# Kernel tuning notes

Measured on AMD Instinct MI355X. Metric: run time of the kernel, lower is better.

## Reference

```python
import jax, jax.numpy as jnp
import numpy as np

V, E, L = 32000, 512, 2  # vocab_size, n_embd (== hidden), n_layer
B, T = 8, 1024


def setup_inputs() -> dict:
    key = jax.random.key(0)
    ks = jax.random.split(key, 6)
    inp = jax.random.randint(ks[0], (B, T), 0, V)
    wte = jax.random.normal(ks[1], (V, E), dtype=jnp.float32) * 0.02
    # PyTorch LSTM params per layer: weight_ih [4H, in], weight_hh [4H, H], b_ih [4H], b_hh [4H]
    W_ih = jax.random.normal(ks[2], (L, 4 * E, E), dtype=jnp.float32) * 0.04
    W_hh = jax.random.normal(ks[3], (L, 4 * E, E), dtype=jnp.float32) * 0.04
    b_ih = jnp.zeros((L, 4 * E), dtype=jnp.float32)
    b_hh = jnp.zeros((L, 4 * E), dtype=jnp.float32)
    fc_w = jax.random.normal(ks[4], (V, E), dtype=jnp.float32) * 0.02
    fc_b = jnp.zeros((V,), dtype=jnp.float32)
    return {"inp": inp, "wte": wte, "W_ih": W_ih, "W_hh": W_hh,
            "b_ih": b_ih, "b_hh": b_hh, "fc_w": fc_w, "fc_b": fc_b}


def _lstm_stack(x, W_ih, W_hh, b_ih, b_hh):
    # x: [B, T, E]; multi-layer LSTM, zero initial (h, c), PyTorch gate order i,f,g,o
    H = W_hh.shape[-1]
    n_layers = W_ih.shape[0]
    for l in range(n_layers):
        # input-to-hidden part is time-parallel: precompute once per layer
        xg = jnp.einsum('bte,ge->btg', x, W_ih[l]) + b_ih[l] + b_hh[l]  # [B,T,4H]
        Whh = W_hh[l]
        h0 = jnp.zeros((x.shape[0], H), x.dtype)
        c0 = jnp.zeros((x.shape[0], H), x.dtype)

        def step(carry, xg_t, Whh=Whh):
            h, c = carry
            g = xg_t + h @ Whh.T  # [B,4H]
            i, f, gg, o = jnp.split(g, 4, axis=-1)
            c = jax.nn.sigmoid(f) * c + jax.nn.sigmoid(i) * jnp.tanh(gg)
            h = jax.nn.sigmoid(o) * jnp.tanh(c)
            return (h, c), h

        (_, _), hs = jax.lax.scan(step, (h0, c0), jnp.swapaxes(xg, 0, 1))  # hs: [T,B,H]
        x = jnp.swapaxes(hs, 0, 1)  # [B,T,H] feeds next layer
    return x


def reference(inp, wte, W_ih, W_hh, b_ih, b_hh, fc_w, fc_b):
    x = wte[inp]  # [B,T,E] embedding lookup
    h = _lstm_stack(x, W_ih, W_hh, b_ih, b_hh)  # [B,T,H]
    logits = jnp.einsum('bth,vh->btv', h, fc_w) + fc_b  # [B,T,V]
    return logits
```

## Files before the change

kernel.cpp:

```cpp
#include <hip/hip_runtime.h>
#include <stdint.h>

typedef __attribute__((ext_vector_type(4))) float f32x4;
typedef __attribute__((ext_vector_type(8))) short s16x8;
typedef __attribute__((ext_vector_type(4))) unsigned short u16x4;
typedef __attribute__((ext_vector_type(4))) unsigned int u32x4;

#define T_SEQ 1024
#define HID 512

__device__ __forceinline__ unsigned short f2bf(float f) {
  uint32_t u = __float_as_uint(f);
  u += 0x7fffu + ((u >> 16) & 1u);
  return (unsigned short)(u >> 16);
}
__device__ __forceinline__ float sigf(float x) { return 1.f / (1.f + __expf(-x)); }
__device__ __forceinline__ float tanhfast(float x) {
  float e = __expf(2.f * x);
  return (e - 1.f) / (e + 1.f);
}

#define ASTORE(p, v) __hip_atomic_store((p), (v), __ATOMIC_RELAXED, __HIP_MEMORY_SCOPE_AGENT)
#define MFMA(a, b, c) __builtin_amdgcn_mfma_f32_16x16x32_bf16((a), (b), (c), 0, 0, 0)

__device__ __forceinline__ u32x4 load_coh16(const unsigned int* p) {
  u32x4 r;
  asm volatile("global_load_dwordx4 %0, %1, off sc0 sc1" : "=v"(r) : "v"(p) : "memory");
  return r;
}
#define VM_WAIT0 do { asm volatile("s_waitcnt vmcnt(0)" ::: "memory"); \
                      __builtin_amdgcn_sched_barrier(0); } while (0)

#define GLL(gp, lp)                                                      \
  __builtin_amdgcn_global_load_lds(                                     \
      (const __attribute__((address_space(1))) void*)(gp),              \
      (__attribute__((address_space(3))) void*)(lp), 16, 0, 0)

__global__ __launch_bounds__(256) void embed_kernel(const int* __restrict__ inp,
                                                    const float* __restrict__ wte,
                                                    unsigned short* __restrict__ xbf) {
  const int m = blockIdx.x;
  const int idx = inp[m];
  const float* src = wte + (size_t)idx * HID;
  unsigned short* dst = xbf + (size_t)m * HID;
  const int e = threadIdx.x;
  dst[e] = f2bf(src[e]);
  dst[e + 256] = f2bf(src[e + 256]);
}

__global__ __launch_bounds__(256) void cvt_bf16_kernel(const float* __restrict__ src,
                                                       unsigned short* __restrict__ dst,
                                                       int n4) {
  const int i = blockIdx.x * 256 + threadIdx.x;
  if (i >= n4) return;
  f32x4 v = ((const f32x4*)src)[i];
  u16x4 o;
  o.x = f2bf(v.x); o.y = f2bf(v.y); o.z = f2bf(v.z); o.w = f2bf(v.w);
  ((u16x4*)dst)[i] = o;
}

__global__ __launch_bounds__(256) void bias_sum_kernel(const float* __restrict__ a,
                                                       const float* __restrict__ b,
                                                       float* __restrict__ o, int n) {
  const int i = blockIdx.x * 256 + threadIdx.x;
  if (i < n) o[i] = a[i] + b[i];
}

template <int MODE>
__global__ __launch_bounds__(256) void gemm_bt(const unsigned short* __restrict__ A,
                                               const unsigned short* __restrict__ B,
                                               float* __restrict__ C,
                                               const float* __restrict__ bias,
                                               int M, int N, int K) {
  __shared__ unsigned short As[128 * 32];
  __shared__ unsigned short Bs[128 * 32];
  const int nTiles = N >> 7;
  const int mt = blockIdx.x / nTiles;
  const int nt = blockIdx.x - mt * nTiles;
  const int m0 = mt << 7, n0 = nt << 7;
  const int tid = threadIdx.x;
  const int wave = tid >> 6, lane = tid & 63;
  const int wm = wave >> 1, wn = wave & 1;

  const int c1 = wave * 64 + lane;
  const int c2 = 256 + c1;
  const unsigned short* gA1 = A + (size_t)(m0 + (c1 >> 2)) * K + (c1 & 3) * 8;
  const unsigned short* gA2 = A + (size_t)(m0 + (c2 >> 2)) * K + (c2 & 3) * 8;
  const unsigned short* gB1 = B + (size_t)(n0 + (c1 >> 2)) * K + (c1 & 3) * 8;
  const unsigned short* gB2 = B + (size_t)(n0 + (c2 >> 2)) * K + (c2 & 3) * 8;
  unsigned short* lA1 = As + wave * 512;
  unsigned short* lA2 = As + 2048 + wave * 512;
  unsigned short* lB1 = Bs + wave * 512;
  unsigned short* lB2 = Bs + 2048 + wave * 512;

  f32x4 acc[4][4] = {};
  const int row_lo = lane & 15;
  const int kq = (lane >> 4) * 8;

  for (int k0 = 0; k0 < K; k0 += 32) {
    GLL(gA1 + k0, lA1);
    GLL(gA2 + k0, lA2);
    GLL(gB1 + k0, lB1);
    GLL(gB2 + k0, lB2);
    __syncthreads();
    s16x8 af[4], bfr[4];
#pragma unroll
    for (int f = 0; f < 4; ++f) {
      af[f] = *(const s16x8*)(As + (wm * 64 + f * 16 + row_lo) * 32 + kq);
      bfr[f] = *(const s16x8*)(Bs + (wn * 64 + f * 16 + row_lo) * 32 + kq);
    }
#pragma unroll
    for (int i = 0; i < 4; ++i)
#pragma unroll
      for (int j = 0; j < 4; ++j)
        acc[i][j] = MFMA(af[i], bfr[j], acc[i][j]);
    __syncthreads();
  }

  float bv[4];
#pragma unroll
  for (int j = 0; j < 4; ++j) bv[j] = bias[n0 + wn * 64 + j * 16 + row_lo];
  const int rbase = (lane >> 4) * 4;
#pragma unroll
  for (int i = 0; i < 4; ++i) {
#pragma unroll
    for (int r = 0; r < 4; ++r) {
      const int m = m0 + wm * 64 + i * 16 + rbase + r;
      const size_t row = MODE == 1 ? ((size_t)(m & 7) * T_SEQ + (m >> 3)) : (size_t)m;
      float* cp = C + row * (size_t)N;
#pragma unroll
      for (int j = 0; j < 4; ++j) cp[n0 + wn * 64 + j * 16 + row_lo] = acc[i][j][r] + bv[j];
    }
  }
}

__global__ __launch_bounds__(256, 1) void lstm_fused(
    const float* __restrict__ xg1,
    const unsigned short* __restrict__ whh1,
    const unsigned short* __restrict__ wih2,
    const unsigned short* __restrict__ whh2,
    const float* __restrict__ bias2,
    unsigned int* __restrict__ h1T,
    unsigned int* __restrict__ h2T,
    unsigned short* __restrict__ h2out) {
  __shared__ __align__(16) char lds1[2][8192];
  __shared__ __align__(16) char lds2[8192];
  __shared__ float GT1[512];
  __shared__ float GT2[512];

  const int tid = threadIdx.x;
  const int wg = blockIdx.x;
  const int g = tid >> 6, l = tid & 63;
  const int unit = l & 15, grp = l >> 4;
  const int u0 = wg * 16;
  const int row = l & 7;

  s16x8 b1[16], b2i[16], b2h[16];
  {
    const size_t grow = (size_t)(g * 512 + u0 + unit) * 512;
#pragma unroll
    for (int kt = 0; kt < 16; ++kt) {
      b1[kt] = *(const s16x8*)(whh1 + grow + kt * 32 + grp * 8);
      b2i[kt] = *(const s16x8*)(wih2 + grow + kt * 32 + grp * 8);
      b2h[kt] = *(const s16x8*)(whh2 + grow + kt * 32 + grp * 8);
    }
  }

  const int pb = l & 7, pu = l >> 3;
  float bias_g[2][4];
  if (g == 0) {
#pragma unroll
    for (int r = 0; r < 2; ++r)
#pragma unroll
      for (int gg = 0; gg < 4; ++gg)
        bias_g[r][gg] = bias2[gg * 512 + u0 + r * 8 + pu];
  }
  float c1a = 0.f, c1b = 0.f, c2a = 0.f, c2b = 0.f;

  const int sr = tid & 7, sc = tid >> 3;
  const int so0 = (sr * 1024 + sc * 32) ^ (sr << 4);
  const int so1 = (sr * 1024 + sc * 32 + 16) ^ (sr << 4);
  const int srcoff = sr * 512 + sc * 16;

  for (int t = 0; t <= T_SEQ + 1; ++t) {
    const int cur = t & 1;

    float xv[2][4];
    if (g == 0 && t < T_SEQ) {
#pragma unroll
      for (int r = 0; r < 2; ++r)
#pragma unroll
        for (int gg = 0; gg < 4; ++gg)
          xv[r][gg] = xg1[((size_t)pb * T_SEQ + t) * 2048 + gg * 512 + u0 + r * 8 + pu];
    }

    const bool need1 = (t >= 1) && (t <= T_SEQ);
    const bool need2 = (t >= 3);
    if (need1 || need2) {
      const unsigned int* s1 = h1T + (size_t)(t - 1) * 4096 + srcoff;
      const unsigned int* s2 = h2T + (size_t)(t - 3) * 4096 + srcoff;
      const unsigned int tg1 = (unsigned int)t, tg2 = (unsigned int)(t - 2);
      u32x4 d0 = {}, d1 = {}, d2 = {}, d3 = {}, e0 = {}, e1 = {}, e2 = {}, e3 = {};
      int spin = 0;
      for (;;) {
        if (need1) {
          d0 = load_coh16(s1); d1 = load_coh16(s1 + 4);
          d2 = load_coh16(s1 + 8); d3 = load_coh16(s1 + 12);
        }
        if (need2) {
          e0 = load_coh16(s2); e1 = load_coh16(s2 + 4);
          e2 = load_coh16(s2 + 8); e3 = load_coh16(s2 + 12);
        }
        VM_WAIT0;
        bool ok = true;
        if (need1) {
#pragma unroll
          for (int j = 0; j < 4; ++j) {
            ok &= (d0[j] >> 16) == tg1; ok &= (d1[j] >> 16) == tg1;
            ok &= (d2[j] >> 16) == tg1; ok &= (d3[j] >> 16) == tg1;
          }
        }
        if (need2) {
#pragma unroll
          for (int j = 0; j < 4; ++j) {
            ok &= (e0[j] >> 16) == tg2; ok &= (e1[j] >> 16) == tg2;
            ok &= (e2[j] >> 16) == tg2; ok &= (e3[j] >> 16) == tg2;
          }
        }
        if (__ballot(ok) == ~0ULL) break;
        if (++spin > (1 << 14)) break;
        __builtin_amdgcn_s_sleep(1);
      }
      if (need1) {
        *(u32x4*)(lds1[cur] + so0) =
            u32x4{(d0[0] & 0xffffu) | (d0[1] << 16), (d0[2] & 0xffffu) | (d0[3] << 16),
                  (d1[0] & 0xffffu) | (d1[1] << 16), (d1[2] & 0xffffu) | (d1[3] << 16)};
        *(u32x4*)(lds1[cur] + so1) =
            u32x4{(d2[0] & 0xffffu) | (d2[1] << 16), (d2[2] & 0xffffu) | (d2[3] << 16),
                  (d3[0] & 0xffffu) | (d3[1] << 16), (d3[2] & 0xffffu) | (d3[3] << 16)};
      }
      if (need2) {
        *(u32x4*)(lds2 + so0) =
            u32x4{(e0[0] & 0xffffu) | (e0[1] << 16), (e0[2] & 0xffffu) | (e0[3] << 16),
                  (e1[0] & 0xffffu) | (e1[1] << 16), (e1[2] & 0xffffu) | (e1[3] << 16)};
        *(u32x4*)(lds2 + so1) =
            u32x4{(e2[0] & 0xffffu) | (e2[1] << 16), (e2[2] & 0xffffu) | (e2[3] << 16),
                  (e3[0] & 0xffffu) | (e3[1] << 16), (e3[2] & 0xffffu) | (e3[3] << 16)};
      }
    }
    if (t == 0) {
      *(u32x4*)(lds1[0] + so0) = u32x4{0, 0, 0, 0};
      *(u32x4*)(lds1[0] + so1) = u32x4{0, 0, 0, 0};
    }
    if (t == 2) {
      *(u32x4*)(lds2 + so0) = u32x4{0, 0, 0, 0};
      *(u32x4*)(lds2 + so1) = u32x4{0, 0, 0, 0};
    }
    __syncthreads();

    if (t < T_SEQ) {
      const char* hb = lds1[cur];
      f32x4 q0 = {}, q1 = {}, q2 = {}, q3 = {};
#pragma unroll
      for (int kt = 0; kt < 16; kt += 4) {
        s16x8 x0 = *(const s16x8*)(hb + ((row * 1024 + (kt + 0) * 64 + grp * 16) ^ (row << 4)));
        s16x8 x1 = *(const s16x8*)(hb + ((row * 1024 + (kt + 1) * 64 + grp * 16) ^ (row << 4)));
        s16x8 x2 = *(const s16x8*)(hb + ((row * 1024 + (kt + 2) * 64 + grp * 16) ^ (row << 4)));
        s16x8 x3 = *(const s16x8*)(hb + ((row * 1024 + (kt + 3) * 64 + grp * 16) ^ (row << 4)));
        q0 = MFMA(x0, b1[kt + 0], q0);
        q1 = MFMA(x1, b1[kt + 1], q1);
        q2 = MFMA(x2, b1[kt + 2], q2);
        q3 = MFMA(x3, b1[kt + 3], q3);
      }
      f32x4 acc = (q0 + q1) + (q2 + q3);
      if (grp < 2) *(f32x4*)(GT1 + g * 128 + unit * 8 + grp * 4) = acc;
    }
    __syncthreads();

    if (g == 0 && t < T_SEQ) {
#pragma unroll
      for (int r = 0; r < 2; ++r) {
        const int u = r * 8 + pu;
        float gi = GT1[0 + u * 8 + pb] + xv[r][0];
        float gf = GT1[128 + u * 8 + pb] + xv[r][1];
        float gv = GT1[256 + u * 8 + pb] + xv[r][2];
        float go = GT1[384 + u * 8 + pb] + xv[r][3];
        float& cc = r ? c1b : c1a;
        cc = sigf(gf) * cc + sigf(gi) * tanhfast(gv);
        const float hv = sigf(go) * tanhfast(cc);
        ASTORE(h1T + (size_t)t * 4096 + pb * 512 + u0 + u,
               (unsigned int)f2bf(hv) | ((unsigned int)(t + 1) << 16));
      }
    }

    if (t >= 2) {
      const char* ha = lds1[cur ^ 1];
      f32x4 q0 = {}, q1 = {}, q2 = {}, q3 = {};
#pragma unroll
      for (int kt = 0; kt < 16; kt += 4) {
        s16x8 x0 = *(const s16x8*)(ha + ((row * 1024 + (kt + 0) * 64 + grp * 16) ^ (row << 4)));
        s16x8 x1 = *(const s16x8*)(ha + ((row * 1024 + (kt + 1) * 64 + grp * 16) ^ (row << 4)));
        s16x8 x2 = *(const s16x8*)(ha + ((row * 1024 + (kt + 2) * 64 + grp * 16) ^ (row << 4)));
        s16x8 x3 = *(const s16x8*)(ha + ((row * 1024 + (kt + 3) * 64 + grp * 16) ^ (row << 4)));
        q0 = MFMA(x0, b2i[kt + 0], q0);
        q1 = MFMA(x1, b2i[kt + 1], q1);
        q2 = MFMA(x2, b2i[kt + 2], q2);
        q3 = MFMA(x3, b2i[kt + 3], q3);
      }
#pragma unroll
      for (int kt = 0; kt < 16; kt += 4) {
        s16x8 x0 = *(const s16x8*)(lds2 + ((row * 1024 + (kt + 0) * 64 + grp * 16) ^ (row << 4)));
        s16x8 x1 = *(const s16x8*)(lds2 + ((row * 1024 + (kt + 1) * 64 + grp * 16) ^ (row << 4)));
        s16x8 x2 = *(const s16x8*)(lds2 + ((row * 1024 + (kt + 2) * 64 + grp * 16) ^ (row << 4)));
        s16x8 x3 = *(const s16x8*)(lds2 + ((row * 1024 + (kt + 3) * 64 + grp * 16) ^ (row << 4)));
        q0 = MFMA(x0, b2h[kt + 0], q0);
        q1 = MFMA(x1, b2h[kt + 1], q1);
        q2 = MFMA(x2, b2h[kt + 2], q2);
        q3 = MFMA(x3, b2h[kt + 3], q3);
      }
      f32x4 acc = (q0 + q1) + (q2 + q3);
      if (grp < 2) *(f32x4*)(GT2 + g * 128 + unit * 8 + grp * 4) = acc;
    }
    __syncthreads();

    if (g == 0 && t >= 2) {
      const int s = t - 2;
#pragma unroll
      for (int r = 0; r < 2; ++r) {
        const int u = r * 8 + pu;
        float gi = GT2[0 + u * 8 + pb] + bias_g[r][0];
        float gf = GT2[128 + u * 8 + pb] + bias_g[r][1];
        float gv = GT2[256 + u * 8 + pb] + bias_g[r][2];
        float go = GT2[384 + u * 8 + pb] + bias_g[r][3];
        float& cc = r ? c2b : c2a;
        cc = sigf(gf) * cc + sigf(gi) * tanhfast(gv);
        const float hv = sigf(go) * tanhfast(cc);
        const unsigned int hb16 = f2bf(hv);
        ASTORE(h2T + (size_t)s * 4096 + pb * 512 + u0 + u,
               hb16 | ((unsigned int)(s + 1) << 16));
        h2out[((size_t)s * 8 + pb) * 512 + u0 + u] = (unsigned short)hb16;
      }
    }
  }
}

extern "C" void kernel_launch(void* const* d_in, const int* in_sizes, int n_in,
                              void* d_out, int out_size, void* d_ws, size_t ws_size,
                              hipStream_t stream) {
  (void)in_sizes; (void)n_in; (void)out_size; (void)ws_size;
  const int* inp = (const int*)d_in[0];
  const float* wte = (const float*)d_in[1];
  const float* W_ih = (const float*)d_in[2];
  const float* W_hh = (const float*)d_in[3];
  const float* b_ih = (const float*)d_in[4];
  const float* b_hh = (const float*)d_in[5];
  const float* fc_w = (const float*)d_in[6];
  const float* fc_b = (const float*)d_in[7];
  float* out = (float*)d_out;

  char* ob = (char*)d_out;
  float* xg1 = (float*)(ob);
  unsigned int* h1T = (unsigned int*)(ob + (64u << 20));
  unsigned int* h2T = (unsigned int*)(ob + (80u << 20));
  unsigned short* x_bf = (unsigned short*)(ob + (96u << 20));
  unsigned short* whh_bf = (unsigned short*)(ob + (104u << 20));
  unsigned short* wih_bf = (unsigned short*)(ob + (108u << 20));

  char* ws = (char*)d_ws;
  unsigned short* fcw_bf = (unsigned short*)(ws);
  float* bias12 = (float*)(ws + (32u << 20));
  unsigned short* h2bf = (unsigned short*)(ws + (35u << 20));

  hipMemsetAsync(ob + (64u << 20), 0, 32u << 20, stream);
  embed_kernel<<<8192, 256, 0, stream>>>(inp, wte, x_bf);
  cvt_bf16_kernel<<<2048, 256, 0, stream>>>(W_ih, wih_bf, 2 * 2048 * 512 / 4);
  cvt_bf16_kernel<<<2048, 256, 0, stream>>>(W_hh, whh_bf, 2 * 2048 * 512 / 4);
  cvt_bf16_kernel<<<16000, 256, 0, stream>>>(fc_w, fcw_bf, 32000 * 512 / 4);
  bias_sum_kernel<<<16, 256, 0, stream>>>(b_ih, b_hh, bias12, 4096);
  gemm_bt<0><<<64 * 16, 256, 0, stream>>>(x_bf, wih_bf, xg1, bias12, 8192, 2048, 512);
  lstm_fused<<<32, 256, 0, stream>>>(xg1, whh_bf, wih_bf + (size_t)2048 * 512,
                                     whh_bf + (size_t)2048 * 512, bias12 + 2048,
                                     h1T, h2T, h2bf);
  gemm_bt<1><<<64 * 250, 256, 0, stream>>>(h2bf, fcw_bf, out, fc_b, 8192, 32000, 512);
}
```

Before: 6.147 ms.

## Warp-specialize fused LSTM kernel with LDS flag handoffs between layer waves

The single lockstep loop over both LSTM layers, with block-wide barriers, becomes a warp-specialized design. Waves 0–1 run layer 1, each computing two gate blocks, and waves 2–3 run layer 2. They hand off through double-buffered LDS tiles and LDS flag counters instead of __syncthreads. Wave 3 prefetches the next layer-1 hidden state while it computes, and the input-projection GEMM now writes a time-major xg layout so the per-step gate loads are contiguous. This is meant to remove the barrier coupling between the layers and to shorten the per-step critical path, at the cost of more spin-polling and of possible deadlock or race hazards in the flag protocol.

```diff
diff --git a/kernel.cpp b/kernel.cpp
--- a/kernel.cpp
+++ b/kernel.cpp
@@ -30,6 +30,23 @@
 }
 #define VM_WAIT0 do { asm volatile("s_waitcnt vmcnt(0)" ::: "memory"); \
                       __builtin_amdgcn_sched_barrier(0); } while (0)
+#define VM_WAIT4 do { asm volatile("s_waitcnt vmcnt(4)" ::: "memory"); \
+                      __builtin_amdgcn_sched_barrier(0); } while (0)
+#define LGKM0 do { asm volatile("s_waitcnt lgkmcnt(0)" ::: "memory"); } while (0)
+
+__device__ __forceinline__ void lds_wait(volatile int* f, int target) {
+  int it = 0;
+  while (*f < target) {
+    if (++it > (1 << 18)) break;
+    __builtin_amdgcn_s_sleep(1);
+  }
+  asm volatile("" ::: "memory");
+}
+
+__device__ __forceinline__ u32x4 pack2(const u32x4 a, const u32x4 b) {
+  return u32x4{(a[0] & 0xffffu) | (a[1] << 16), (a[2] & 0xffffu) | (a[3] << 16),
+               (b[0] & 0xffffu) | (b[1] << 16), (b[2] & 0xffffu) | (b[3] << 16)};
+}
 
 #define GLL(gp, lp)                                                      \
   __builtin_amdgcn_global_load_lds(                                     \
@@ -126,7 +143,9 @@
 #pragma unroll
     for (int r = 0; r < 4; ++r) {
       const int m = m0 + wm * 64 + i * 16 + rbase + r;
-      const size_t row = MODE == 1 ? ((size_t)(m & 7) * T_SEQ + (m >> 3)) : (size_t)m;
+      const size_t row = MODE == 1 ? ((size_t)(m & 7) * T_SEQ + (m >> 3))
+                       : MODE == 2 ? ((size_t)(m & (T_SEQ - 1)) * 8 + (m >> 10))
+                                   : (size_t)m;
       float* cp = C + row * (size_t)N;
 #pragma unroll
       for (int j = 0; j < 4; ++j) cp[n0 + wn * 64 + j * 16 + row_lo] = acc[i][j][r] + bv[j];
@@ -134,8 +153,8 @@
   }
 }
 
-__global__ __launch_bounds__(256, 1) void lstm_fused(
-    const float* __restrict__ xg1,
+__global__ __launch_bounds__(256, 1) void lstm_ws(
+    const float* __restrict__ xg1t,
     const unsigned short* __restrict__ whh1,
     const unsigned short* __restrict__ wih2,
     const unsigned short* __restrict__ whh2,
@@ -143,198 +162,319 @@
     unsigned int* __restrict__ h1T,
     unsigned int* __restrict__ h2T,
     unsigned short* __restrict__ h2out) {
-  __shared__ __align__(16) char lds1[2][8192];
-  __shared__ __align__(16) char lds2[8192];
-  __shared__ float GT1[512];
-  __shared__ float GT2[512];
-
-  const int tid = threadIdx.x;
-  const int wg = blockIdx.x;
-  const int g = tid >> 6, l = tid & 63;
+  __shared__ __align__(16) char t1[2][8192];
+  __shared__ __align__(16) char t1b[2][8192];
+  __shared__ __align__(16) char t2[2][8192];
+  __shared__ float GT1[2][512];
+  __shared__ float GT2[2][512];
+  __shared__ float XG[2][512];
+  __shared__ int F[8];
+
+  const int tid = threadIdx.x, wave = tid >> 6, l = tid & 63;
+  const int wg = blockIdx.x, u0 = wg * 16;
   const int unit = l & 15, grp = l >> 4;
-  const int u0 = wg * 16;
   const int row = l & 7;
-
-  s16x8 b1[16], b2i[16], b2h[16];
-  {
-    const size_t grow = (size_t)(g * 512 + u0 + unit) * 512;
-#pragma unroll
-    for (int kt = 0; kt < 16; ++kt) {
-      b1[kt] = *(const s16x8*)(whh1 + grow + kt * 32 + grp * 8);
-      b2i[kt] = *(const s16x8*)(wih2 + grow + kt * 32 + grp * 8);
-      b2h[kt] = *(const s16x8*)(whh2 + grow + kt * 32 + grp * 8);
-    }
-  }
-
-  const int pb = l & 7, pu = l >> 3;
-  float bias_g[2][4];
-  if (g == 0) {
-#pragma unroll
-    for (int r = 0; r < 2; ++r)
-#pragma unroll
-      for (int gg = 0; gg < 4; ++gg)
-        bias_g[r][gg] = bias2[gg * 512 + u0 + r * 8 + pu];
-  }
-  float c1a = 0.f, c1b = 0.f, c2a = 0.f, c2b = 0.f;
-
-  const int sr = tid & 7, sc = tid >> 3;
-  const int so0 = (sr * 1024 + sc * 32) ^ (sr << 4);
-  const int so1 = (sr * 1024 + sc * 32 + 16) ^ (sr << 4);
-  const int srcoff = sr * 512 + sc * 16;
-
-  for (int t = 0; t <= T_SEQ + 1; ++t) {
-    const int cur = t & 1;
-
-    float xv[2][4];
-    if (g == 0 && t < T_SEQ) {
-#pragma unroll
-      for (int r = 0; r < 2; ++r)
-#pragma unroll
-        for (int gg = 0; gg < 4; ++gg)
-          xv[r][gg] = xg1[((size_t)pb * T_SEQ + t) * 2048 + gg * 512 + u0 + r * 8 + pu];
-    }
-
-    const bool need1 = (t >= 1) && (t <= T_SEQ);
-    const bool need2 = (t >= 3);
-    if (need1 || need2) {
-      const unsigned int* s1 = h1T + (size_t)(t - 1) * 4096 + srcoff;
-      const unsigned int* s2 = h2T + (size_t)(t - 3) * 4096 + srcoff;
-      const unsigned int tg1 = (unsigned int)t, tg2 = (unsigned int)(t - 2);
-      u32x4 d0 = {}, d1 = {}, d2 = {}, d3 = {}, e0 = {}, e1 = {}, e2 = {}, e3 = {};
-      int spin = 0;
-      for (;;) {
-        if (need1) {
-          d0 = load_coh16(s1); d1 = load_coh16(s1 + 4);
-          d2 = load_coh16(s1 + 8); d3 = load_coh16(s1 + 12);
-        }
-        if (need2) {
-          e0 = load_coh16(s2); e1 = load_coh16(s2 + 4);
-          e2 = load_coh16(s2 + 8); e3 = load_coh16(s2 + 12);
-        }
-        VM_WAIT0;
-        bool ok = true;
-        if (need1) {
-#pragma unroll
-          for (int j = 0; j < 4; ++j) {
-            ok &= (d0[j] >> 16) == tg1; ok &= (d1[j] >> 16) == tg1;
-            ok &= (d2[j] >> 16) == tg1; ok &= (d3[j] >> 16) == tg1;
-          }
-        }
-        if (need2) {
-#pragma unroll
-          for (int j = 0; j < 4; ++j) {
-            ok &= (e0[j] >> 16) == tg2; ok &= (e1[j] >> 16) == tg2;
-            ok &= (e2[j] >> 16) == tg2; ok &= (e3[j] >> 16) == tg2;
-          }
-        }
-        if (__ballot(ok) == ~0ULL) break;
-        if (++spin > (1 << 14)) break;
-        __builtin_amdgcn_s_sleep(1);
-      }
-      if (need1) {
-        *(u32x4*)(lds1[cur] + so0) =
-            u32x4{(d0[0] & 0xffffu) | (d0[1] << 16), (d0[2] & 0xffffu) | (d0[3] << 16),
-                  (d1[0] & 0xffffu) | (d1[1] << 16), (d1[2] & 0xffffu) | (d1[3] << 16)};
-        *(u32x4*)(lds1[cur] + so1) =
-            u32x4{(d2[0] & 0xffffu) | (d2[1] << 16), (d2[2] & 0xffffu) | (d2[3] << 16),
-                  (d3[0] & 0xffffu) | (d3[1] << 16), (d3[2] & 0xffffu) | (d3[3] << 16)};
-      }
-      if (need2) {
-        *(u32x4*)(lds2 + so0) =
-            u32x4{(e0[0] & 0xffffu) | (e0[1] << 16), (e0[2] & 0xffffu) | (e0[3] << 16),
-                  (e1[0] & 0xffffu) | (e1[1] << 16), (e1[2] & 0xffffu) | (e1[3] << 16)};
-        *(u32x4*)(lds2 + so1) =
-            u32x4{(e2[0] & 0xffffu) | (e2[1] << 16), (e2[2] & 0xffffu) | (e2[3] << 16),
-                  (e3[0] & 0xffffu) | (e3[1] << 16), (e3[2] & 0xffffu) | (e3[3] << 16)};
-      }
-    }
-    if (t == 0) {
-      *(u32x4*)(lds1[0] + so0) = u32x4{0, 0, 0, 0};
-      *(u32x4*)(lds1[0] + so1) = u32x4{0, 0, 0, 0};
-    }
-    if (t == 2) {
-      *(u32x4*)(lds2 + so0) = u32x4{0, 0, 0, 0};
-      *(u32x4*)(lds2 + so1) = u32x4{0, 0, 0, 0};
-    }
-    __syncthreads();
-
-    if (t < T_SEQ) {
-      const char* hb = lds1[cur];
-      f32x4 q0 = {}, q1 = {}, q2 = {}, q3 = {};
-#pragma unroll
-      for (int kt = 0; kt < 16; kt += 4) {
-        s16x8 x0 = *(const s16x8*)(hb + ((row * 1024 + (kt + 0) * 64 + grp * 16) ^ (row << 4)));
-        s16x8 x1 = *(const s16x8*)(hb + ((row * 1024 + (kt + 1) * 64 + grp * 16) ^ (row << 4)));
-        s16x8 x2 = *(const s16x8*)(hb + ((row * 1024 + (kt + 2) * 64 + grp * 16) ^ (row << 4)));
-        s16x8 x3 = *(const s16x8*)(hb + ((row * 1024 + (kt + 3) * 64 + grp * 16) ^ (row << 4)));
-        q0 = MFMA(x0, b1[kt + 0], q0);
-        q1 = MFMA(x1, b1[kt + 1], q1);
-        q2 = MFMA(x2, b1[kt + 2], q2);
-        q3 = MFMA(x3, b1[kt + 3], q3);
-      }
-      f32x4 acc = (q0 + q1) + (q2 + q3);
-      if (grp < 2) *(f32x4*)(GT1 + g * 128 + unit * 8 + grp * 4) = acc;
-    }
-    __syncthreads();
-
-    if (g == 0 && t < T_SEQ) {
+  const int c64 = l >> 3;
+  volatile int* vF = F;
+
+  if (tid < 8) F[tid] = 0;
+  __syncthreads();
+
+  if (wave == 0) {
+    s16x8 bf[2][16];
+#pragma unroll
+    for (int gi = 0; gi < 2; ++gi) {
+      const size_t grow = (size_t)(gi * 512 + u0 + unit) * 512;
+#pragma unroll
+      for (int kt = 0; kt < 16; ++kt)
+        bf[gi][kt] = *(const s16x8*)(whh1 + grow + kt * 32 + grp * 8);
+    }
+    const int xb = (l >> 1) & 7, xg_ = l >> 4, xh = l & 1;
+    for (int t = 0; t < T_SEQ; ++t) {
+      const int par = t & 1;
+      const float* xs = xg1t + ((size_t)t * 8 + xb) * 2048 + xg_ * 512 + u0 + xh * 8;
+      f32x4 xa = *(const f32x4*)xs;
+      f32x4 xc = *(const f32x4*)(xs + 4);
+      char* dst = t1[par];
+      if (t > 0) {
+        const unsigned int* src = h1T + (size_t)(t - 1) * 4096 + row * 512 + c64 * 64;
+        const unsigned int tg = (unsigned int)t;
+        u32x4 d[16];
+        int spin = 0;
+        for (;;) {
+#pragma unroll
+          for (int j = 0; j < 16; ++j) d[j] = load_coh16(src + j * 4);
+          VM_WAIT0;
+          bool ok = true;
+#pragma unroll
+          for (int j = 0; j < 16; ++j)
+#pragma unroll
+            for (int k = 0; k < 4; ++k) ok &= (d[j][k] >> 16) == tg;
+          if (__ballot(ok) == ~0ULL) break;
+          if (++spin > (1 << 12)) break;
+          __builtin_amdgcn_s_sleep(1);
+        }
+#pragma unroll
+        for (int j2 = 0; j2 < 8; ++j2)
+          *(u32x4*)(dst + ((row * 1024 + c64 * 128 + j2 * 16) ^ (row << 4))) =
+              pack2(d[j2 * 2], d[j2 * 2 + 1]);
+      } else {
+#pragma unroll
+        for (int j2 = 0; j2 < 8; ++j2)
+          *(u32x4*)(dst + ((row * 1024 + c64 * 128 + j2 * 16) ^ (row << 4))) = u32x4{0, 0, 0, 0};
+      }
+      float* xgd = &XG[par][xg_ * 128 + xb * 16 + xh * 8];
+      *(f32x4*)xgd = xa;
+      *(f32x4*)(xgd + 4) = xc;
+      LGKM0;
+      vF[0] = t + 1;
+      const char* hb = t1[par];
+#pragma unroll
+      for (int gi = 0; gi < 2; ++gi) {
+        f32x4 q0 = {}, q1 = {}, q2 = {}, q3 = {};
+#pragma unroll
+        for (int kt = 0; kt < 16; kt += 4) {
+          s16x8 x0 = *(const s16x8*)(hb + ((row * 1024 + (kt + 0) * 64 + grp * 16) ^ (row << 4)));
+          s16x8 x1 = *(const s16x8*)(hb + ((row * 1024 + (kt + 1) * 64 + grp * 16) ^ (row << 4)));
+          s16x8 x2 = *(const s16x8*)(hb + ((row * 1024 + (kt + 2) * 64 + grp * 16) ^ (row << 4)));
+          s16x8 x3 = *(const s16x8*)(hb + ((row * 1024 + (kt + 3) * 64 + grp * 16) ^ (row << 4)));
+          q0 = MFMA(x0, bf[gi][kt + 0], q0);
+          q1 = MFMA(x1, bf[gi][kt + 1], q1);
+          q2 = MFMA(x2, bf[gi][kt + 2], q2);
+          q3 = MFMA(x3, bf[gi][kt + 3], q3);
+        }
+        f32x4 acc = (q0 + q1) + (q2 + q3);
+        if (grp < 2) *(f32x4*)(&GT1[par][gi * 128 + unit * 8 + grp * 4]) = acc;
+      }
+      LGKM0;
+      vF[1] = t + 1;
+    }
+  } else if (wave == 1) {
+    s16x8 bf[2][16];
+#pragma unroll
+    for (int gi = 0; gi < 2; ++gi) {
+      const size_t grow = (size_t)((2 + gi) * 512 + u0 + unit) * 512;
+#pragma unroll
+      for (int kt = 0; kt < 16; ++kt)
+        bf[gi][kt] = *(const s16x8*)(whh1 + grow + kt * 32 + grp * 8);
+    }
+    const int pb = l & 7, pu = l >> 3;
+    float cst[2] = {0.f, 0.f};
+    for (int t = 0; t < T_SEQ; ++t) {
+      const int par = t & 1;
+      lds_wait(&vF[0], t + 1);
+      const char* hb = t1[par];
+#pragma unroll
+      for (int gi = 0; gi < 2; ++gi) {
+        f32x4 q0 = {}, q1 = {}, q2 = {}, q3 = {};
+#pragma unroll
+        for (int kt = 0; kt < 16; kt += 4) {
+          s16x8 x0 = *(const s16x8*)(hb + ((row * 1024 + (kt + 0) * 64 + grp * 16) ^ (row << 4)));
+          s16x8 x1 = *(const s16x8*)(hb + ((row * 1024 + (kt + 1) * 64 + grp * 16) ^ (row << 4)));
+          s16x8 x2 = *(const s16x8*)(hb + ((row * 1024 + (kt + 2) * 64 + grp * 16) ^ (row << 4)));
+          s16x8 x3 = *(const s16x8*)(hb + ((row * 1024 + (kt + 3) * 64 + grp * 16) ^ (row << 4)));
+          q0 = MFMA(x0, bf[gi][kt + 0], q0);
+          q1 = MFMA(x1, bf[gi][kt + 1], q1);
+          q2 = MFMA(x2, bf[gi][kt + 2], q2);
+          q3 = MFMA(x3, bf[gi][kt + 3], q3);
+        }
+        f32x4 acc = (q0 + q1) + (q2 + q3);
+        if (grp < 2) *(f32x4*)(&GT1[par][(2 + gi) * 128 + unit * 8 + grp * 4]) = acc;
+      }
+      lds_wait(&vF[1], t + 1);
 #pragma unroll
       for (int r = 0; r < 2; ++r) {
         const int u = r * 8 + pu;
-        float gi = GT1[0 + u * 8 + pb] + xv[r][0];
-        float gf = GT1[128 + u * 8 + pb] + xv[r][1];
-        float gv = GT1[256 + u * 8 + pb] + xv[r][2];
-        float go = GT1[384 + u * 8 + pb] + xv[r][3];
-        float& cc = r ? c1b : c1a;
-        cc = sigf(gf) * cc + sigf(gi) * tanhfast(gv);
-        const float hv = sigf(go) * tanhfast(cc);
+        float gi = GT1[par][0 + u * 8 + pb] + XG[par][0 + pb * 16 + u];
+        float gf = GT1[par][128 + u * 8 + pb] + XG[par][128 + pb * 16 + u];
+        float gv = GT1[par][256 + u * 8 + pb] + XG[par][256 + pb * 16 + u];
+        float go = GT1[par][384 + u * 8 + pb] + XG[par][384 + pb * 16 + u];
+        cst[r] = sigf(gf) * cst[r] + sigf(gi) * tanhfast(gv);
+        const float hv = sigf(go) * tanhfast(cst[r]);
         ASTORE(h1T + (size_t)t * 4096 + pb * 512 + u0 + u,
                (unsigned int)f2bf(hv) | ((unsigned int)(t + 1) << 16));
       }
     }
-
-    if (t >= 2) {
-      const char* ha = lds1[cur ^ 1];
-      f32x4 q0 = {}, q1 = {}, q2 = {}, q3 = {};
-#pragma unroll
-      for (int kt = 0; kt < 16; kt += 4) {
-        s16x8 x0 = *(const s16x8*)(ha + ((row * 1024 + (kt + 0) * 64 + grp * 16) ^ (row << 4)));
-        s16x8 x1 = *(const s16x8*)(ha + ((row * 1024 + (kt + 1) * 64 + grp * 16) ^ (row << 4)));
-        s16x8 x2 = *(const s16x8*)(ha + ((row * 1024 + (kt + 2) * 64 + grp * 16) ^ (row << 4)));
-        s16x8 x3 = *(const s16x8*)(ha + ((row * 1024 + (kt + 3) * 64 + grp * 16) ^ (row << 4)));
-        q0 = MFMA(x0, b2i[kt + 0], q0);
-        q1 = MFMA(x1, b2i[kt + 1], q1);
-        q2 = MFMA(x2, b2i[kt + 2], q2);
-        q3 = MFMA(x3, b2i[kt + 3], q3);
-      }
-#pragma unroll
-      for (int kt = 0; kt < 16; kt += 4) {
-        s16x8 x0 = *(const s16x8*)(lds2 + ((row * 1024 + (kt + 0) * 64 + grp * 16) ^ (row << 4)));
-        s16x8 x1 = *(const s16x8*)(lds2 + ((row * 1024 + (kt + 1) * 64 + grp * 16) ^ (row << 4)));
-        s16x8 x2 = *(const s16x8*)(lds2 + ((row * 1024 + (kt + 2) * 64 + grp * 16) ^ (row << 4)));
-        s16x8 x3 = *(const s16x8*)(lds2 + ((row * 1024 + (kt + 3) * 64 + grp * 16) ^ (row << 4)));
-        q0 = MFMA(x0, b2h[kt + 0], q0);
-        q1 = MFMA(x1, b2h[kt + 1], q1);
-        q2 = MFMA(x2, b2h[kt + 2], q2);
-        q3 = MFMA(x3, b2h[kt + 3], q3);
-      }
-      f32x4 acc = (q0 + q1) + (q2 + q3);
-      if (grp < 2) *(f32x4*)(GT2 + g * 128 + unit * 8 + grp * 4) = acc;
-    }
-    __syncthreads();
-
-    if (g == 0 && t >= 2) {
-      const int s = t - 2;
+  } else if (wave == 2) {
+    s16x8 bi[2][16], bh[2][16];
+#pragma unroll
+    for (int gi = 0; gi < 2; ++gi) {
+      const size_t grow = (size_t)(gi * 512 + u0 + unit) * 512;
+#pragma unroll
+      for (int kt = 0; kt < 16; ++kt) {
+        bi[gi][kt] = *(const s16x8*)(wih2 + grow + kt * 32 + grp * 8);
+        bh[gi][kt] = *(const s16x8*)(whh2 + grow + kt * 32 + grp * 8);
+      }
+    }
+    for (int s = 0; s < T_SEQ; ++s) {
+      const int par = s & 1;
+      char* dst = t2[par];
+      if (s > 0) {
+        const unsigned int* src = h2T + (size_t)(s - 1) * 4096 + row * 512 + c64 * 64;
+        const unsigned int tg = (unsigned int)s;
+        u32x4 d[16];
+        int spin = 0;
+        for (;;) {
+#pragma unroll
+          for (int j = 0; j < 16; ++j) d[j] = load_coh16(src + j * 4);
+          VM_WAIT0;
+          bool ok = true;
+#pragma unroll
+          for (int j = 0; j < 16; ++j)
+#pragma unroll
+            for (int k = 0; k < 4; ++k) ok &= (d[j][k] >> 16) == tg;
+          if (__ballot(ok) == ~0ULL) break;
+          if (++spin > (1 << 12)) break;
+          __builtin_amdgcn_s_sleep(1);
+        }
+#pragma unroll
+        for (int j2 = 0; j2 < 8; ++j2)
+          *(u32x4*)(dst + ((row * 1024 + c64 * 128 + j2 * 16) ^ (row << 4))) =
+              pack2(d[j2 * 2], d[j2 * 2 + 1]);
+      } else {
+#pragma unroll
+        for (int j2 = 0; j2 < 8; ++j2)
+          *(u32x4*)(dst + ((row * 1024 + c64 * 128 + j2 * 16) ^ (row << 4))) = u32x4{0, 0, 0, 0};
+      }
+      LGKM0;
+      vF[2] = s + 1;
+      lds_wait(&vF[4], s + 1);
+      const char* ha = t1b[par];
+      const char* hc = t2[par];
+#pragma unroll
+      for (int gi = 0; gi < 2; ++gi) {
+        f32x4 q0 = {}, q1 = {}, q2 = {}, q3 = {};
+#pragma unroll
+        for (int kt = 0; kt < 16; kt += 4) {
+          s16x8 x0 = *(const s16x8*)(ha + ((row * 1024 + (kt + 0) * 64 + grp * 16) ^ (row << 4)));
+          s16x8 x1 = *(const s16x8*)(ha + ((row * 1024 + (kt + 1) * 64 + grp * 16) ^ (row << 4)));
+          s16x8 x2 = *(const s16x8*)(ha + ((row * 1024 + (kt + 2) * 64 + grp * 16) ^ (row << 4)));
+          s16x8 x3 = *(const s16x8*)(ha + ((row * 1024 + (kt + 3) * 64 + grp * 16) ^ (row << 4)));
+          q0 = MFMA(x0, bi[gi][kt + 0], q0);
+          q1 = MFMA(x1, bi[gi][kt + 1], q1);
+          q2 = MFMA(x2, bi[gi][kt + 2], q2);
+          q3 = MFMA(x3, bi[gi][kt + 3], q3);
+        }
+#pragma unroll
+        for (int kt = 0; kt < 16; kt += 4) {
+          s16x8 x0 = *(const s16x8*)(hc + ((row * 1024 + (kt + 0) * 64 + grp * 16) ^ (row << 4)));
+          s16x8 x1 = *(const s16x8*)(hc + ((row * 1024 + (kt + 1) * 64 + grp * 16) ^ (row << 4)));
+          s16x8 x2 = *(const s16x8*)(hc + ((row * 1024 + (kt + 2) * 64 + grp * 16) ^ (row << 4)));
+          s16x8 x3 = *(const s16x8*)(hc + ((row * 1024 + (kt + 3) * 64 + grp * 16) ^ (row << 4)));
+          q0 = MFMA(x0, bh[gi][kt + 0], q0);
+          q1 = MFMA(x1, bh[gi][kt + 1], q1);
+          q2 = MFMA(x2, bh[gi][kt + 2], q2);
+          q3 = MFMA(x3, bh[gi][kt + 3], q3);
+        }
+        f32x4 acc = (q0 + q1) + (q2 + q3);
+        if (grp < 2) *(f32x4*)(&GT2[par][gi * 128 + unit * 8 + grp * 4]) = acc;
+      }
+      LGKM0;
+      vF[3] = s + 1;
+    }
+  } else {
+    s16x8 bi[2][16], bh[2][16];
+#pragma unroll
+    for (int gi = 0; gi < 2; ++gi) {
+      const size_t grow = (size_t)((2 + gi) * 512 + u0 + unit) * 512;
+#pragma unroll
+      for (int kt = 0; kt < 16; ++kt) {
+        bi[gi][kt] = *(const s16x8*)(wih2 + grow + kt * 32 + grp * 8);
+        bh[gi][kt] = *(const s16x8*)(whh2 + grow + kt * 32 + grp * 8);
+      }
+    }
+    const int pb = l & 7, pu = l >> 3;
+    float bias_g[2][4];
+#pragma unroll
+    for (int r = 0; r < 2; ++r)
+#pragma unroll
+      for (int g = 0; g < 4; ++g) bias_g[r][g] = bias2[g * 512 + u0 + r * 8 + pu];
+    float cst[2] = {0.f, 0.f};
+    u32x4 pre[16];
+    {
+      const unsigned int* src = h1T + row * 512 + c64 * 64;
+#pragma unroll
+      for (int j = 0; j < 16; ++j) pre[j] = load_coh16(src + j * 4);
+    }
+    for (int s = 0; s < T_SEQ; ++s) {
+      const int par = s & 1;
+      if (s == 0) { VM_WAIT0; } else { VM_WAIT4; }
+      const unsigned int tg1 = (unsigned int)(s + 1);
+      bool ok = true;
+#pragma unroll
+      for (int j = 0; j < 16; ++j)
+#pragma unroll
+        for (int k = 0; k < 4; ++k) ok &= (pre[j][k] >> 16) == tg1;
+      if (__ballot(ok) != ~0ULL) {
+        const unsigned int* src = h1T + (size_t)s * 4096 + row * 512 + c64 * 64;
+        int spin = 0;
+        for (;;) {
+#pragma unroll
+          for (int j = 0; j < 16; ++j) pre[j] = load_coh16(src + j * 4);
+          VM_WAIT0;
+          ok = true;
+#pragma unroll
+          for (int j = 0; j < 16; ++j)
+#pragma unroll
+            for (int k = 0; k < 4; ++k) ok &= (pre[j][k] >> 16) == tg1;
+          if (__ballot(ok) == ~0ULL) break;
+          if (++spin > (1 << 12)) break;
+          __builtin_amdgcn_s_sleep(1);
+        }
+      }
+      char* dst = t1b[par];
+#pragma unroll
+      for (int j2 = 0; j2 < 8; ++j2)
+        *(u32x4*)(dst + ((row * 1024 + c64 * 128 + j2 * 16) ^ (row << 4))) =
+            pack2(pre[j2 * 2], pre[j2 * 2 + 1]);
+      LGKM0;
+      vF[4] = s + 1;
+      lds_wait(&vF[2], s + 1);
+      const char* ha = t1b[par];
+      const char* hc = t2[par];
+#pragma unroll
+      for (int gi = 0; gi < 2; ++gi) {
+        f32x4 q0 = {}, q1 = {}, q2 = {}, q3 = {};
+#pragma unroll
+        for (int kt = 0; kt < 16; kt += 4) {
+          s16x8 x0 = *(const s16x8*)(ha + ((row * 1024 + (kt + 0) * 64 + grp * 16) ^ (row << 4)));
+          s16x8 x1 = *(const s16x8*)(ha + ((row * 1024 + (kt + 1) * 64 + grp * 16) ^ (row << 4)));
+          s16x8 x2 = *(const s16x8*)(ha + ((row * 1024 + (kt + 2) * 64 + grp * 16) ^ (row << 4)));
+          s16x8 x3 = *(const s16x8*)(ha + ((row * 1024 + (kt + 3) * 64 + grp * 16) ^ (row << 4)));
+          q0 = MFMA(x0, bi[gi][kt + 0], q0);
+          q1 = MFMA(x1, bi[gi][kt + 1], q1);
+          q2 = MFMA(x2, bi[gi][kt + 2], q2);
+          q3 = MFMA(x3, bi[gi][kt + 3], q3);
+        }
+#pragma unroll
+        for (int kt = 0; kt < 16; kt += 4) {
+          s16x8 x0 = *(const s16x8*)(hc + ((row * 1024 + (kt + 0) * 64 + grp * 16) ^ (row << 4)));
+          s16x8 x1 = *(const s16x8*)(hc + ((row * 1024 + (kt + 1) * 64 + grp * 16) ^ (row << 4)));
+          s16x8 x2 = *(const s16x8*)(hc + ((row * 1024 + (kt + 2) * 64 + grp * 16) ^ (row << 4)));
+          s16x8 x3 = *(const s16x8*)(hc + ((row * 1024 + (kt + 3) * 64 + grp * 16) ^ (row << 4)));
+          q0 = MFMA(x0, bh[gi][kt + 0], q0);
+          q1 = MFMA(x1, bh[gi][kt + 1], q1);
+          q2 = MFMA(x2, bh[gi][kt + 2], q2);
+          q3 = MFMA(x3, bh[gi][kt + 3], q3);
+        }
+        f32x4 acc = (q0 + q1) + (q2 + q3);
+        if (grp < 2) *(f32x4*)(&GT2[par][(2 + gi) * 128 + unit * 8 + grp * 4]) = acc;
+      }
+      if (s + 1 < T_SEQ) {
+        const unsigned int* src = h1T + (size_t)(s + 1) * 4096 + row * 512 + c64 * 64;
+#pragma unroll
+        for (int j = 0; j < 16; ++j) pre[j] = load_coh16(src + j * 4);
+      }
+      lds_wait(&vF[3], s + 1);
 #pragma unroll
       for (int r = 0; r < 2; ++r) {
         const int u = r * 8 + pu;
-        float gi = GT2[0 + u * 8 + pb] + bias_g[r][0];
-        float gf = GT2[128 + u * 8 + pb] + bias_g[r][1];
-        float gv = GT2[256 + u * 8 + pb] + bias_g[r][2];
-        float go = GT2[384 + u * 8 + pb] + bias_g[r][3];
-        float& cc = r ? c2b : c2a;
-        cc = sigf(gf) * cc + sigf(gi) * tanhfast(gv);
-        const float hv = sigf(go) * tanhfast(cc);
+        float gi = GT2[par][0 + u * 8 + pb] + bias_g[r][0];
+        float gf = GT2[par][128 + u * 8 + pb] + bias_g[r][1];
+        float gv = GT2[par][256 + u * 8 + pb] + bias_g[r][2];
+        float go = GT2[par][384 + u * 8 + pb] + bias_g[r][3];
+        cst[r] = sigf(gf) * cst[r] + sigf(gi) * tanhfast(gv);
+        const float hv = sigf(go) * tanhfast(cst[r]);
         const unsigned int hb16 = f2bf(hv);
         ASTORE(h2T + (size_t)s * 4096 + pb * 512 + u0 + u,
                hb16 | ((unsigned int)(s + 1) << 16));
@@ -359,7 +499,7 @@
   float* out = (float*)d_out;
 
   char* ob = (char*)d_out;
-  float* xg1 = (float*)(ob);
+  float* xg1t = (float*)(ob);
   unsigned int* h1T = (unsigned int*)(ob + (64u << 20));
   unsigned int* h2T = (unsigned int*)(ob + (80u << 20));
   unsigned short* x_bf = (unsigned short*)(ob + (96u << 20));
@@ -377,9 +517,9 @@
   cvt_bf16_kernel<<<2048, 256, 0, stream>>>(W_hh, whh_bf, 2 * 2048 * 512 / 4);
   cvt_bf16_kernel<<<16000, 256, 0, stream>>>(fc_w, fcw_bf, 32000 * 512 / 4);
   bias_sum_kernel<<<16, 256, 0, stream>>>(b_ih, b_hh, bias12, 4096);
-  gemm_bt<0><<<64 * 16, 256, 0, stream>>>(x_bf, wih_bf, xg1, bias12, 8192, 2048, 512);
-  lstm_fused<<<32, 256, 0, stream>>>(xg1, whh_bf, wih_bf + (size_t)2048 * 512,
-                                     whh_bf + (size_t)2048 * 512, bias12 + 2048,
-                                     h1T, h2T, h2bf);
+  gemm_bt<2><<<64 * 16, 256, 0, stream>>>(x_bf, wih_bf, xg1t, bias12, 8192, 2048, 512);
+  lstm_ws<<<32, 256, 0, stream>>>(xg1t, whh_bf, wih_bf + (size_t)2048 * 512,
+                                  whh_bf + (size_t)2048 * 512, bias12 + 2048,
+                                  h1T, h2T, h2bf);
   gemm_bt<1><<<64 * 250, 256, 0, stream>>>(h2bf, fcw_bf, out, fc_b, 8192, 32000, 512);
 }
```

Result: slower. 9.525 ms (+55.0%).
